# Kernel optimization log

Measured on AMD Instinct MI355X. Metric: run time of the kernel, lower is better.

## Reference

```python
import jax, jax.numpy as jnp
import numpy as np

N, L, D, H = 4, 2048, 1024, 16
HD = D // H  # head_dim = 64


def setup_inputs() -> dict:
    key = jax.random.key(0)
    ks = jax.random.split(key, 6)
    x = jax.random.normal(ks[0], (N, L, D), dtype=jnp.float32)
    mask = jax.random.randint(ks[1], (N, L), 0, 2).astype(bool)
    W_qkv = jax.random.normal(ks[2], (3 * D, D), dtype=jnp.float32) * (1.0 / np.sqrt(D))
    b_qkv = jax.random.normal(ks[3], (3 * D,), dtype=jnp.float32) * 0.02
    W_out = jax.random.normal(ks[4], (D, D), dtype=jnp.float32) * (1.0 / np.sqrt(D))
    b_out = jax.random.normal(ks[5], (D,), dtype=jnp.float32) * 0.02
    return {"x": x, "mask": mask, "W_qkv": W_qkv, "b_qkv": b_qkv,
            "W_out": W_out, "b_out": b_out}


def reference(x, mask, W_qkv, b_qkv, W_out, b_out):
    # qkv projection: torch Linear is y = x @ W.T + b
    qkv = jnp.einsum('nld,ed->nle', x, W_qkv) + b_qkv          # [N, L, 3D]
    q, k, v = jnp.split(qkv, 3, axis=-1)                        # each [N, L, D]
    # [N, L, D] -> [N, H, L, HD]
    to_heads = lambda t: t.reshape(N, L, H, HD).transpose(0, 2, 1, 3)
    q, k, v = to_heads(q), to_heads(k), to_heads(v)
    scale = 1.0 / np.sqrt(HD)
    scores = jnp.einsum('nhqd,nhkd->nhqk', q, k) * scale        # [N, H, L, L]
    # faithful to source: masked_fill where mask is True -> -1e9
    scores = jnp.where(mask[:, None, None, :], -1e9, scores)
    attn = jax.nn.softmax(scores, axis=-1)                      # dropout = identity (eval)
    out = jnp.einsum('nhqk,nhkd->nhqd', attn, v)                # [N, H, L, HD]
    out = out.transpose(0, 2, 1, 3).reshape(N, L, D)
    return jnp.einsum('nld,ed->nle', out, W_out) + b_out
```

## Files before the change

### kernel.cpp

```cpp
#include <hip/hip_runtime.h>
#include <hip/hip_bf16.h>
#include <cmath>

#define NB   4
#define LL   2048
#define DD   1024
#define HH   16
#define HD   64

typedef __bf16 bf16;
typedef __bf16 bf16x4 __attribute__((ext_vector_type(4)));
typedef __bf16 bf16x8 __attribute__((ext_vector_type(8)));
typedef float  f32x4  __attribute__((ext_vector_type(4)));
typedef float  f32x8  __attribute__((ext_vector_type(8)));

__device__ __forceinline__ void gload16(void* lds_base, const void* gsrc) {
    __builtin_amdgcn_global_load_lds(
        (const __attribute__((address_space(1))) unsigned int*)gsrc,
        (__attribute__((address_space(3))) unsigned int*)lds_base, 16, 0, 0);
}

__global__ __launch_bounds__(1024) void mask_prep(const unsigned char* __restrict__ mraw,
                                                  float* __restrict__ maskB) {
    __shared__ int anyOdd;
    if (threadIdx.x == 0) anyOdd = 0;
    __syncthreads();
    const int base = blockIdx.x * 1024;
    const int i = base + threadIdx.x;
    if ((i & 3) != 0 && mraw[i] != 0) atomicOr(&anyOdd, 1);
    __syncthreads();
    const bool isBytes = (anyOdd != 0);
    int v = isBytes ? (int)mraw[i] : ((const int*)mraw)[i];
    maskB[i] = v ? -1.4426950408889634e9f : -12.0f;
}

__global__ __launch_bounds__(256) void cast_f32_bf16(const float* __restrict__ src,
                                                     bf16* __restrict__ dst, int n8) {
    const int i = blockIdx.x * 256 + threadIdx.x;
    if (i >= n8) return;
    const float4* s = (const float4*)src + (size_t)i * 2;
    float4 a = s[0], b = s[1];
    bf16x8 o;
    o[0] = (bf16)a.x; o[1] = (bf16)a.y; o[2] = (bf16)a.z; o[3] = (bf16)a.w;
    o[4] = (bf16)b.x; o[5] = (bf16)b.y; o[6] = (bf16)b.z; o[7] = (bf16)b.w;
    *((bf16x8*)dst + i) = o;
}

template <int EPI>
__global__ __launch_bounds__(256) void gemm_mfma(const bf16* __restrict__ A,
                                                 const bf16* __restrict__ B,
                                                 const float* __restrict__ bias,
                                                 void* __restrict__ C0v,
                                                 void* __restrict__ C1v,
                                                 void* __restrict__ C2v,
                                                 int M, int N, int K) {
    __shared__ __attribute__((aligned(16))) char As[128 * 64];
    __shared__ __attribute__((aligned(16))) char Bs[128 * 64];

    const int tid = threadIdx.x;
    const int wave = tid >> 6;
    const int lane = tid & 63;
    const int kl = lane & 15;
    const int h = lane >> 4;
    const int wm = wave >> 1;
    const int wn = wave & 1;
    const int m0 = blockIdx.y * 128;
    const int n0 = blockIdx.x * 128;

    f32x4 acc[4][4];
#pragma unroll
    for (int i = 0; i < 4; ++i)
#pragma unroll
        for (int j = 0; j < 4; ++j) acc[i][j] = (f32x4){0.f, 0.f, 0.f, 0.f};

    const int sr = wave * 16 + (lane >> 2);
    const int sc = (lane & 3) * 16;
    const char* A0 = (const char*)A + ((size_t)(m0 + sr) * K) * 2 + sc;
    const char* A1 = (const char*)A + ((size_t)(m0 + 64 + sr) * K) * 2 + sc;
    const char* B0 = (const char*)B + ((size_t)(n0 + sr) * K) * 2 + sc;
    const char* B1 = (const char*)B + ((size_t)(n0 + 64 + sr) * K) * 2 + sc;
    char* AsD = As + wave * 1024;
    char* BsD = Bs + wave * 1024;

    for (int kt = 0; kt < K; kt += 32) {
        __syncthreads();
        gload16(AsD,        A0 + kt * 2);
        gload16(AsD + 4096, A1 + kt * 2);
        gload16(BsD,        B0 + kt * 2);
        gload16(BsD + 4096, B1 + kt * 2);
        asm volatile("s_waitcnt vmcnt(0)" ::: "memory");
        __syncthreads();

        bf16x8 a[4], b[4];
#pragma unroll
        for (int mt = 0; mt < 4; ++mt)
            a[mt] = *(const bf16x8*)(As + (wm * 64 + mt * 16 + kl) * 64 + h * 16);
#pragma unroll
        for (int nt = 0; nt < 4; ++nt)
            b[nt] = *(const bf16x8*)(Bs + (wn * 64 + nt * 16 + kl) * 64 + h * 16);
#pragma unroll
        for (int mt = 0; mt < 4; ++mt)
#pragma unroll
            for (int nt = 0; nt < 4; ++nt)
                acc[mt][nt] = __builtin_amdgcn_mfma_f32_16x16x32_bf16(a[mt], b[nt], acc[mt][nt], 0, 0, 0);
    }

    if (EPI == 1) {
        float* C0 = (float*)C0v;
#pragma unroll
        for (int mt = 0; mt < 4; ++mt) {
            const int mb = m0 + wm * 64 + mt * 16 + 4 * h;
#pragma unroll
            for (int nt = 0; nt < 4; ++nt) {
                const int n = n0 + wn * 64 + nt * 16 + kl;
                const float bv = bias[n];
#pragma unroll
                for (int r = 0; r < 4; ++r)
                    C0[(size_t)(mb + r) * N + n] = acc[mt][nt][r] + bv;
            }
        }
    } else {
        const int which = n0 >> 10;
        if (which < 2) {
            bf16* dst = (which == 0) ? (bf16*)C0v : (bf16*)C1v;
#pragma unroll
            for (int mt = 0; mt < 4; ++mt) {
                const int mb = m0 + wm * 64 + mt * 16 + 4 * h;
#pragma unroll
                for (int nt = 0; nt < 4; ++nt) {
                    const int gn = n0 + wn * 64 + nt * 16 + kl;
                    const float bv = bias[gn];
                    const int nn = gn & 1023;
                    const int hh = nn >> 6;
                    const int d = nn & 63;
#pragma unroll
                    for (int r = 0; r < 4; ++r) {
                        const int m = mb + r;
                        const int n_ = m >> 11;
                        const int l_ = m & 2047;
                        dst[((size_t)(n_ * HH + hh) * LL + l_) * HD + d] = (bf16)(acc[mt][nt][r] + bv);
                    }
                }
            }
        } else {
            bf16* dst = (bf16*)C2v;
#pragma unroll
            for (int mt = 0; mt < 4; ++mt) {
                const int mb = m0 + wm * 64 + mt * 16 + 4 * h;
                const int n_ = mb >> 11;
                const int l0 = mb & 2047;
#pragma unroll
                for (int nt = 0; nt < 4; ++nt) {
                    const int gn = n0 + wn * 64 + nt * 16 + kl;
                    const float bv = bias[gn];
                    const int nn = gn & 1023;
                    const int hh = nn >> 6;
                    const int d = nn & 63;
                    bf16x4 o4;
#pragma unroll
                    for (int r = 0; r < 4; ++r) o4[r] = (bf16)(acc[mt][nt][r] + bv);
                    *(bf16x4*)(dst + ((size_t)(n_ * HH + hh) * HD + d) * LL + l0) = o4;
                }
            }
        }
    }
}

#define SWZ3(row) ((((row) & 3) | ((((row) >> 3) & 1) << 2)) << 4)

__global__ __launch_bounds__(256) void attn_mfma(const bf16* __restrict__ Qg,
                                                 const bf16* __restrict__ Kg,
                                                 const bf16* __restrict__ VTg,
                                                 const float* __restrict__ maskB,
                                                 bf16* __restrict__ Oout) {
    __shared__ __attribute__((aligned(16))) char KtB0[8192];
    __shared__ __attribute__((aligned(16))) char KtB1[8192];
    __shared__ __attribute__((aligned(16))) char VtB0[8192];
    __shared__ __attribute__((aligned(16))) char VtB1[8192];

    const int tid = threadIdx.x;
    const int wave = tid >> 6;
    const int lane = tid & 63;
    const int kl = lane & 15;
    const int h = lane >> 4;

    const int f = blockIdx.x;
    const int qb = (f >> 3) & 15;
    const int bh = (f & 7) + ((f >> 7) << 3);
    const int n_ = bh >> 4;
    const int hh = bh & 15;
    const int q0 = qb * 128 + wave * 32;

    bf16x8 qf[2][2];
#pragma unroll
    for (int qt = 0; qt < 2; ++qt)
#pragma unroll
        for (int st = 0; st < 2; ++st)
            qf[qt][st] = *(const bf16x8*)(Qg + (((size_t)bh * LL + q0 + qt * 16 + kl) * HD + st * 32 + h * 8));

    f32x4 Oa[2][4];
    f32x4 Osum[2];
#pragma unroll
    for (int qt = 0; qt < 2; ++qt) {
        Osum[qt] = (f32x4){0.f, 0.f, 0.f, 0.f};
#pragma unroll
        for (int t = 0; t < 4; ++t) Oa[qt][t] = (f32x4){0.f, 0.f, 0.f, 0.f};
    }

    bf16x8 ones;
#pragma unroll
    for (int j = 0; j < 8; ++j) ones[j] = (bf16)1.0f;

    int koff[2][2][2];
#pragma unroll
    for (int c = 0; c < 2; ++c) {
        const int r1 = c * 32 + ((kl >> 2) << 3) + (kl & 3);
        const int r2 = r1 + 4;
#pragma unroll
        for (int st = 0; st < 2; ++st) {
            koff[c][0][st] = r1 * 128 + ((st * 64 + h * 16) ^ SWZ3(r1));
            koff[c][1][st] = r2 * 128 + ((st * 64 + h * 16) ^ SWZ3(r2));
        }
    }
    int voff[2][4];
#pragma unroll
    for (int c = 0; c < 2; ++c)
#pragma unroll
        for (int tt = 0; tt < 4; ++tt) {
            const int row = tt * 16 + kl;
            voff[c][tt] = row * 128 + ((c * 64 + h * 16) ^ SWZ3(row));
        }

    const int i0 = wave * 2 + 0, i1 = wave * 2 + 1;
    const int rA = i0 * 8 + (lane >> 3);
    const int rB = i1 * 8 + (lane >> 3);
    const int swA = ((lane & 7) << 4) ^ SWZ3(rA);
    const int swB = ((lane & 7) << 4) ^ SWZ3(rB);
    const char* Kb = (const char*)Kg + (size_t)bh * LL * 128;
    const char* Vb = (const char*)VTg + (size_t)bh * HD * (LL * 2);
    const char* kSA = Kb + (size_t)rA * 128 + swA;
    const char* kSB = Kb + (size_t)rB * 128 + swB;
    const char* vSA = Vb + (size_t)rA * 4096 + swA;
    const char* vSB = Vb + (size_t)rB * 4096 + swB;

    const float* mptr = maskB + n_ * LL + h * 8;
    const float scale = 0.18033688011f;

#define STAGE_TO(KT, VT, k0s)                                 \
    do {                                                      \
        gload16((KT) + i0 * 1024, kSA + (size_t)(k0s) * 128); \
        gload16((KT) + i1 * 1024, kSB + (size_t)(k0s) * 128); \
        gload16((VT) + i0 * 1024, vSA + (k0s) * 2);           \
        gload16((VT) + i1 * 1024, vSB + (k0s) * 2);           \
    } while (0)

#define LOADMK(MK, k0s)                                                    \
    do {                                                                   \
        _Pragma("unroll") for (int c = 0; c < 2; ++c)                      \
            _Pragma("unroll") for (int f2 = 0; f2 < 2; ++f2)               \
                MK[c][f2] = *(const f32x4*)(mptr + (k0s) + c * 32 + f2 * 4); \
    } while (0)

#define COMPUTE(KT, VT, MK)                                                            \
    do {                                                                               \
        bf16x8 kf[2][2][2], vf[2][4];                                                  \
        _Pragma("unroll") for (int c = 0; c < 2; ++c) {                                \
            _Pragma("unroll") for (int fr = 0; fr < 2; ++fr)                           \
                _Pragma("unroll") for (int st = 0; st < 2; ++st)                       \
                    kf[c][fr][st] = *(const bf16x8*)((KT) + koff[c][fr][st]);          \
            _Pragma("unroll") for (int tt = 0; tt < 4; ++tt)                           \
                vf[c][tt] = *(const bf16x8*)((VT) + voff[c][tt]);                      \
        }                                                                              \
        asm volatile("s_waitcnt lgkmcnt(0)" ::: "memory");                             \
        __builtin_amdgcn_sched_barrier(0);                                             \
        _Pragma("unroll") for (int qt = 0; qt < 2; ++qt) {                             \
            f32x4 sv[2][2];                                                            \
            __builtin_amdgcn_s_setprio(1);                                             \
            _Pragma("unroll") for (int c = 0; c < 2; ++c)                              \
                _Pragma("unroll") for (int fr = 0; fr < 2; ++fr) {                     \
                    f32x4 z = {0.f, 0.f, 0.f, 0.f};                                    \
                    f32x4 a = __builtin_amdgcn_mfma_f32_16x16x32_bf16(kf[c][fr][0],    \
                                                         qf[qt][0], z, 0, 0, 0);       \
                    sv[c][fr] = __builtin_amdgcn_mfma_f32_16x16x32_bf16(kf[c][fr][1],  \
                                                         qf[qt][1], a, 0, 0, 0);       \
                }                                                                      \
            __builtin_amdgcn_s_setprio(0);                                             \
            bf16x8 pa[2];                                                              \
            _Pragma("unroll") for (int c = 0; c < 2; ++c) {                            \
                f32x8 pf;                                                              \
                _Pragma("unroll") for (int f2 = 0; f2 < 2; ++f2) {                     \
                    f32x4 s = sv[c][f2] * scale + MK[c][f2];                           \
                    _Pragma("unroll") for (int r = 0; r < 4; ++r)                      \
                        pf[f2 * 4 + r] = __builtin_amdgcn_exp2f(s[r]);                 \
                }                                                                      \
                pa[c] = __builtin_convertvector(pf, bf16x8);                           \
            }                                                                          \
            __builtin_amdgcn_s_setprio(1);                                             \
            Osum[qt] = __builtin_amdgcn_mfma_f32_16x16x32_bf16(pa[0], ones,            \
                                                               Osum[qt], 0, 0, 0);     \
            Osum[qt] = __builtin_amdgcn_mfma_f32_16x16x32_bf16(pa[1], ones,            \
                                                               Osum[qt], 0, 0, 0);     \
            _Pragma("unroll") for (int c = 0; c < 2; ++c)                              \
                _Pragma("unroll") for (int tt = 0; tt < 4; ++tt)                       \
                    Oa[qt][tt] = __builtin_amdgcn_mfma_f32_16x16x32_bf16(pa[c],        \
                                                 vf[c][tt], Oa[qt][tt], 0, 0, 0);      \
            __builtin_amdgcn_s_setprio(0);                                             \
        }                                                                              \
    } while (0)

    f32x4 mkA[2][2], mkB[2][2];

    LOADMK(mkA, 0);
    STAGE_TO(KtB0, VtB0, 0);
    asm volatile("s_waitcnt vmcnt(0)" ::: "memory");
    __builtin_amdgcn_s_barrier();

    for (int t = 0; t < 32; t += 2) {
        STAGE_TO(KtB1, VtB1, (t + 1) * 64);
        __builtin_amdgcn_sched_barrier(0);
        LOADMK(mkB, (t + 1) * 64);
        COMPUTE(KtB0, VtB0, mkA);
        asm volatile("s_waitcnt vmcnt(4)" ::: "memory");
        __builtin_amdgcn_s_barrier();

        if (t + 2 < 32) {
            STAGE_TO(KtB0, VtB0, (t + 2) * 64);
            __builtin_amdgcn_sched_barrier(0);
            LOADMK(mkA, (t + 2) * 64);
            COMPUTE(KtB1, VtB1, mkB);
            asm volatile("s_waitcnt vmcnt(4)" ::: "memory");
            __builtin_amdgcn_s_barrier();
        } else {
            COMPUTE(KtB1, VtB1, mkB);
        }
    }

#pragma unroll
    for (int qt = 0; qt < 2; ++qt) {
#pragma unroll
        for (int r = 0; r < 4; ++r) {
            const float inv = 1.0f / Osum[qt][r];
            const int qrow = q0 + qt * 16 + h * 4 + r;
#pragma unroll
            for (int tt = 0; tt < 4; ++tt)
                Oout[((size_t)n_ * LL + qrow) * DD + hh * HD + tt * 16 + kl] =
                    (bf16)(Oa[qt][tt][r] * inv);
        }
    }
#undef STAGE_TO
#undef LOADMK
#undef COMPUTE
}

extern "C" void kernel_launch(void* const* d_in, const int* in_sizes, int n_in,
                              void* d_out, int out_size, void* d_ws, size_t ws_size,
                              hipStream_t stream) {
    const float* x     = (const float*)d_in[0];
    const void*  mask  = d_in[1];
    const float* W_qkv = (const float*)d_in[2];
    const float* b_qkv = (const float*)d_in[3];
    const float* W_out = (const float*)d_in[4];
    const float* b_out = (const float*)d_in[5];
    float* out = (float*)d_out;

    char* ws = (char*)d_ws;
    float* maskB = (float*)ws;
    bf16*  xb    = (bf16*)(ws + (1ull  << 20));
    bf16*  wqb   = (bf16*)(ws + (18ull << 20));
    bf16*  wob   = (bf16*)(ws + (25ull << 20));
    bf16*  qb    = (bf16*)(ws + (28ull << 20));
    bf16*  kb    = (bf16*)(ws + (45ull << 20));
    bf16*  vtb   = (bf16*)(ws + (62ull << 20));
    bf16*  attnb = (bf16*)(ws + (79ull << 20));

    mask_prep<<<8, 1024, 0, stream>>>((const unsigned char*)mask, maskB);

    cast_f32_bf16<<<(NB * LL * DD / 8) / 256, 256, 0, stream>>>(x, xb, NB * LL * DD / 8);
    cast_f32_bf16<<<(3 * DD * DD / 8) / 256, 256, 0, stream>>>(W_qkv, wqb, 3 * DD * DD / 8);
    cast_f32_bf16<<<(DD * DD / 8) / 256, 256, 0, stream>>>(W_out, wob, DD * DD / 8);

    gemm_mfma<0><<<dim3(3 * DD / 128, NB * LL / 128), 256, 0, stream>>>(
        xb, wqb, b_qkv, qb, kb, vtb, NB * LL, 3 * DD, DD);

    attn_mfma<<<1024, 256, 0, stream>>>(qb, kb, vtb, maskB, attnb);

    gemm_mfma<1><<<dim3(DD / 128, NB * LL / 128), 256, 0, stream>>>(
        attnb, wob, b_out, out, nullptr, nullptr, NB * LL, DD, DD);
}
```

Baseline: 214.4 us.

## Widen attention blocks to 8 waves and split K/V LDS read waits

The attention kernel now runs 512 threads per block covering 256 query rows, so each staged K/V tile serves twice as many queries. Each wave now issues one K load and one V load per stage instead of two of each. Inside COMPUTE, the K fragment reads come first and only they are waited on (lgkmcnt(8)) before the QK MFMAs and exp; the V reads are awaited later, before the PV MFMAs. The s_setprio hints are removed. The larger blocks halve the grid to 512 blocks, which may reduce occupancy and load balance across CUs.

Result: faster. 208.1 us (-2.9%).

```diff
diff --git a/kernel.cpp b/kernel.cpp
--- a/kernel.cpp
+++ b/kernel.cpp
@@ -168,7 +168,7 @@
 
 #define SWZ3(row) ((((row) & 3) | ((((row) >> 3) & 1) << 2)) << 4)
 
-__global__ __launch_bounds__(256) void attn_mfma(const bf16* __restrict__ Qg,
+__global__ __launch_bounds__(512) void attn_mfma(const bf16* __restrict__ Qg,
                                                  const bf16* __restrict__ Kg,
                                                  const bf16* __restrict__ VTg,
                                                  const float* __restrict__ maskB,
@@ -185,11 +185,11 @@
     const int h = lane >> 4;
 
     const int f = blockIdx.x;
-    const int qb = (f >> 3) & 15;
-    const int bh = (f & 7) + ((f >> 7) << 3);
+    const int qb = (f >> 3) & 7;
+    const int bh = (f & 7) | ((f >> 6) << 3);
     const int n_ = bh >> 4;
     const int hh = bh & 15;
-    const int q0 = qb * 128 + wave * 32;
+    const int q0 = qb * 256 + wave * 32;
 
     bf16x8 qf[2][2];
 #pragma unroll
@@ -231,51 +231,45 @@
             voff[c][tt] = row * 128 + ((c * 64 + h * 16) ^ SWZ3(row));
         }
 
-    const int i0 = wave * 2 + 0, i1 = wave * 2 + 1;
-    const int rA = i0 * 8 + (lane >> 3);
-    const int rB = i1 * 8 + (lane >> 3);
+    const int rA = wave * 8 + (lane >> 3);
     const int swA = ((lane & 7) << 4) ^ SWZ3(rA);
-    const int swB = ((lane & 7) << 4) ^ SWZ3(rB);
     const char* Kb = (const char*)Kg + (size_t)bh * LL * 128;
     const char* Vb = (const char*)VTg + (size_t)bh * HD * (LL * 2);
     const char* kSA = Kb + (size_t)rA * 128 + swA;
-    const char* kSB = Kb + (size_t)rB * 128 + swB;
     const char* vSA = Vb + (size_t)rA * 4096 + swA;
-    const char* vSB = Vb + (size_t)rB * 4096 + swB;
 
     const float* mptr = maskB + n_ * LL + h * 8;
     const float scale = 0.18033688011f;
 
-#define STAGE_TO(KT, VT, k0s)                                 \
-    do {                                                      \
-        gload16((KT) + i0 * 1024, kSA + (size_t)(k0s) * 128); \
-        gload16((KT) + i1 * 1024, kSB + (size_t)(k0s) * 128); \
-        gload16((VT) + i0 * 1024, vSA + (k0s) * 2);           \
-        gload16((VT) + i1 * 1024, vSB + (k0s) * 2);           \
+#define STAGE_TO(KT, VT, k0s)                                   \
+    do {                                                        \
+        gload16((KT) + wave * 1024, kSA + (size_t)(k0s) * 128); \
+        gload16((VT) + wave * 1024, vSA + (k0s) * 2);           \
     } while (0)
 
-#define LOADMK(MK, k0s)                                                    \
-    do {                                                                   \
-        _Pragma("unroll") for (int c = 0; c < 2; ++c)                      \
-            _Pragma("unroll") for (int f2 = 0; f2 < 2; ++f2)               \
+#define LOADMK(MK, k0s)                                                      \
+    do {                                                                     \
+        _Pragma("unroll") for (int c = 0; c < 2; ++c)                        \
+            _Pragma("unroll") for (int f2 = 0; f2 < 2; ++f2)                 \
                 MK[c][f2] = *(const f32x4*)(mptr + (k0s) + c * 32 + f2 * 4); \
     } while (0)
 
 #define COMPUTE(KT, VT, MK)                                                            \
     do {                                                                               \
         bf16x8 kf[2][2][2], vf[2][4];                                                  \
-        _Pragma("unroll") for (int c = 0; c < 2; ++c) {                                \
+        _Pragma("unroll") for (int c = 0; c < 2; ++c)                                  \
             _Pragma("unroll") for (int fr = 0; fr < 2; ++fr)                           \
                 _Pragma("unroll") for (int st = 0; st < 2; ++st)                       \
                     kf[c][fr][st] = *(const bf16x8*)((KT) + koff[c][fr][st]);          \
+        __builtin_amdgcn_sched_barrier(0);             \
+        _Pragma("unroll") for (int c = 0; c < 2; ++c)                                  \
             _Pragma("unroll") for (int tt = 0; tt < 4; ++tt)                           \
                 vf[c][tt] = *(const bf16x8*)((VT) + voff[c][tt]);                      \
-        }                                                                              \
-        asm volatile("s_waitcnt lgkmcnt(0)" ::: "memory");                             \
+        asm volatile("s_waitcnt lgkmcnt(8)" ::: "memory");                \
         __builtin_amdgcn_sched_barrier(0);                                             \
+        bf16x8 pa[2][2];                                                               \
         _Pragma("unroll") for (int qt = 0; qt < 2; ++qt) {                             \
             f32x4 sv[2][2];                                                            \
-            __builtin_amdgcn_s_setprio(1);                                             \
             _Pragma("unroll") for (int c = 0; c < 2; ++c)                              \
                 _Pragma("unroll") for (int fr = 0; fr < 2; ++fr) {                     \
                     f32x4 z = {0.f, 0.f, 0.f, 0.f};                                    \
@@ -284,8 +278,6 @@
                     sv[c][fr] = __builtin_amdgcn_mfma_f32_16x16x32_bf16(kf[c][fr][1],  \
                                                          qf[qt][1], a, 0, 0, 0);       \
                 }                                                                      \
-            __builtin_amdgcn_s_setprio(0);                                             \
-            bf16x8 pa[2];                                                              \
             _Pragma("unroll") for (int c = 0; c < 2; ++c) {                            \
                 f32x8 pf;                                                              \
                 _Pragma("unroll") for (int f2 = 0; f2 < 2; ++f2) {                     \
@@ -293,18 +285,20 @@
                     _Pragma("unroll") for (int r = 0; r < 4; ++r)                      \
                         pf[f2 * 4 + r] = __builtin_amdgcn_exp2f(s[r]);                 \
                 }                                                                      \
-                pa[c] = __builtin_convertvector(pf, bf16x8);                           \
+                pa[qt][c] = __builtin_convertvector(pf, bf16x8);                       \
             }                                                                          \
-            __builtin_amdgcn_s_setprio(1);                                             \
-            Osum[qt] = __builtin_amdgcn_mfma_f32_16x16x32_bf16(pa[0], ones,            \
+        }                                                                              \
+        asm volatile("s_waitcnt lgkmcnt(0)" ::: "memory");                \
+        __builtin_amdgcn_sched_barrier(0);                                             \
+        _Pragma("unroll") for (int qt = 0; qt < 2; ++qt) {                             \
+            Osum[qt] = __builtin_amdgcn_mfma_f32_16x16x32_bf16(pa[qt][0], ones,        \
                                                                Osum[qt], 0, 0, 0);     \
-            Osum[qt] = __builtin_amdgcn_mfma_f32_16x16x32_bf16(pa[1], ones,            \
+            Osum[qt] = __builtin_amdgcn_mfma_f32_16x16x32_bf16(pa[qt][1], ones,        \
                                                                Osum[qt], 0, 0, 0);     \
             _Pragma("unroll") for (int c = 0; c < 2; ++c)                              \
                 _Pragma("unroll") for (int tt = 0; tt < 4; ++tt)                       \
-                    Oa[qt][tt] = __builtin_amdgcn_mfma_f32_16x16x32_bf16(pa[c],        \
+                    Oa[qt][tt] = __builtin_amdgcn_mfma_f32_16x16x32_bf16(pa[qt][c],    \
                                                  vf[c][tt], Oa[qt][tt], 0, 0, 0);      \
-            __builtin_amdgcn_s_setprio(0);                                             \
         }                                                                              \
     } while (0)
 
@@ -382,7 +376,7 @@
     gemm_mfma<0><<<dim3(3 * DD / 128, NB * LL / 128), 256, 0, stream>>>(
         xb, wqb, b_qkv, qb, kb, vtb, NB * LL, 3 * DD, DD);
 
-    attn_mfma<<<1024, 256, 0, stream>>>(qb, kb, vtb, maskB, attnb);
+    attn_mfma<<<512, 512, 0, stream>>>(qb, kb, vtb, maskB, attnb);
 
     gemm_mfma<1><<<dim3(DD / 128, NB * LL / 128), 256, 0, stream>>>(
         attnb, wob, b_out, out, nullptr, nullptr, NB * LL, DD, DD);
```

## Double attention query tile per wave, stage mask in LDS, batch PV phase

Applied to the files above, without the earlier changes.

Each wave now handles 64 query rows instead of 32 (256 per block), halving the grid to 512 blocks so each K/V tile loaded into LDS is reused across twice as many queries. The per-batch mask row is preloaded once into LDS instead of being read from global memory every iteration. The compute is restructured to run all QK^T and softmax for four query tiles first, then load V fragments and do all PV MFMAs, and the setprio hints are dropped. The cost is higher register pressure, fewer blocks for occupancy, and a stricter vmcnt(0) wait each step.

Measured after the change: 219.4 us. +2.4%, slower.

```diff
diff --git a/kernel.cpp b/kernel.cpp
--- a/kernel.cpp
+++ b/kernel.cpp
@@ -177,6 +177,7 @@
     __shared__ __attribute__((aligned(16))) char KtB1[8192];
     __shared__ __attribute__((aligned(16))) char VtB0[8192];
     __shared__ __attribute__((aligned(16))) char VtB1[8192];
+    __shared__ __attribute__((aligned(16))) char MaskL[8192];
 
     const int tid = threadIdx.x;
     const int wave = tid >> 6;
@@ -185,23 +186,23 @@
     const int h = lane >> 4;
 
     const int f = blockIdx.x;
-    const int qb = (f >> 3) & 15;
-    const int bh = (f & 7) + ((f >> 7) << 3);
+    const int qb = (f >> 3) & 7;
+    const int bh = (f & 7) | ((f >> 6) << 3);
     const int n_ = bh >> 4;
     const int hh = bh & 15;
-    const int q0 = qb * 128 + wave * 32;
-
-    bf16x8 qf[2][2];
-#pragma unroll
-    for (int qt = 0; qt < 2; ++qt)
+    const int q0 = qb * 256 + wave * 64;
+
+    bf16x8 qf[4][2];
+#pragma unroll
+    for (int qt = 0; qt < 4; ++qt)
 #pragma unroll
         for (int st = 0; st < 2; ++st)
             qf[qt][st] = *(const bf16x8*)(Qg + (((size_t)bh * LL + q0 + qt * 16 + kl) * HD + st * 32 + h * 8));
 
-    f32x4 Oa[2][4];
-    f32x4 Osum[2];
-#pragma unroll
-    for (int qt = 0; qt < 2; ++qt) {
+    f32x4 Oa[4][4];
+    f32x4 Osum[4];
+#pragma unroll
+    for (int qt = 0; qt < 4; ++qt) {
         Osum[qt] = (f32x4){0.f, 0.f, 0.f, 0.f};
 #pragma unroll
         for (int t = 0; t < 4; ++t) Oa[qt][t] = (f32x4){0.f, 0.f, 0.f, 0.f};
@@ -243,8 +244,8 @@
     const char* vSA = Vb + (size_t)rA * 4096 + swA;
     const char* vSB = Vb + (size_t)rB * 4096 + swB;
 
-    const float* mptr = maskB + n_ * LL + h * 8;
     const float scale = 0.18033688011f;
+    const char* mlds = MaskL + h * 32;
 
 #define STAGE_TO(KT, VT, k0s)                                 \
     do {                                                      \
@@ -254,28 +255,22 @@
         gload16((VT) + i1 * 1024, vSB + (k0s) * 2);           \
     } while (0)
 
-#define LOADMK(MK, k0s)                                                    \
-    do {                                                                   \
-        _Pragma("unroll") for (int c = 0; c < 2; ++c)                      \
-            _Pragma("unroll") for (int f2 = 0; f2 < 2; ++f2)               \
-                MK[c][f2] = *(const f32x4*)(mptr + (k0s) + c * 32 + f2 * 4); \
-    } while (0)
-
-#define COMPUTE(KT, VT, MK)                                                            \
+#define COMPUTE(KT, VT, MOFF)                                                          \
     do {                                                                               \
-        bf16x8 kf[2][2][2], vf[2][4];                                                  \
-        _Pragma("unroll") for (int c = 0; c < 2; ++c) {                                \
+        bf16x8 kf[2][2][2];                                                            \
+        _Pragma("unroll") for (int c = 0; c < 2; ++c)                                  \
             _Pragma("unroll") for (int fr = 0; fr < 2; ++fr)                           \
                 _Pragma("unroll") for (int st = 0; st < 2; ++st)                       \
                     kf[c][fr][st] = *(const bf16x8*)((KT) + koff[c][fr][st]);          \
-            _Pragma("unroll") for (int tt = 0; tt < 4; ++tt)                           \
-                vf[c][tt] = *(const bf16x8*)((VT) + voff[c][tt]);                      \
-        }                                                                              \
-        asm volatile("s_waitcnt lgkmcnt(0)" ::: "memory");                             \
         __builtin_amdgcn_sched_barrier(0);                                             \
-        _Pragma("unroll") for (int qt = 0; qt < 2; ++qt) {                             \
+        f32x4 mk[2][2];                                                                \
+        _Pragma("unroll") for (int c = 0; c < 2; ++c)                                  \
+            _Pragma("unroll") for (int f2 = 0; f2 < 2; ++f2)                           \
+                mk[c][f2] = *(const f32x4*)(mlds + (MOFF) + c * 128 + f2 * 16);        \
+        __builtin_amdgcn_sched_barrier(0);                                             \
+        bf16x8 pa[4][2];                                                               \
+        _Pragma("unroll") for (int qt = 0; qt < 4; ++qt) {                             \
             f32x4 sv[2][2];                                                            \
-            __builtin_amdgcn_s_setprio(1);                                             \
             _Pragma("unroll") for (int c = 0; c < 2; ++c)                              \
                 _Pragma("unroll") for (int fr = 0; fr < 2; ++fr) {                     \
                     f32x4 z = {0.f, 0.f, 0.f, 0.f};                                    \
@@ -284,33 +279,38 @@
                     sv[c][fr] = __builtin_amdgcn_mfma_f32_16x16x32_bf16(kf[c][fr][1],  \
                                                          qf[qt][1], a, 0, 0, 0);       \
                 }                                                                      \
-            __builtin_amdgcn_s_setprio(0);                                             \
-            bf16x8 pa[2];                                                              \
             _Pragma("unroll") for (int c = 0; c < 2; ++c) {                            \
                 f32x8 pf;                                                              \
                 _Pragma("unroll") for (int f2 = 0; f2 < 2; ++f2) {                     \
-                    f32x4 s = sv[c][f2] * scale + MK[c][f2];                           \
+                    f32x4 s = sv[c][f2] * scale + mk[c][f2];                           \
                     _Pragma("unroll") for (int r = 0; r < 4; ++r)                      \
                         pf[f2 * 4 + r] = __builtin_amdgcn_exp2f(s[r]);                 \
                 }                                                                      \
-                pa[c] = __builtin_convertvector(pf, bf16x8);                           \
+                pa[qt][c] = __builtin_convertvector(pf, bf16x8);                       \
             }                                                                          \
-            __builtin_amdgcn_s_setprio(1);                                             \
-            Osum[qt] = __builtin_amdgcn_mfma_f32_16x16x32_bf16(pa[0], ones,            \
+        }                                                                              \
+        __builtin_amdgcn_sched_barrier(0);                                             \
+        bf16x8 vf[2][4];                                                               \
+        _Pragma("unroll") for (int c = 0; c < 2; ++c)                                  \
+            _Pragma("unroll") for (int tt = 0; tt < 4; ++tt)                           \
+                vf[c][tt] = *(const bf16x8*)((VT) + voff[c][tt]);                      \
+        _Pragma("unroll") for (int qt = 0; qt < 4; ++qt) {                             \
+            Osum[qt] = __builtin_amdgcn_mfma_f32_16x16x32_bf16(pa[qt][0], ones,        \
                                                                Osum[qt], 0, 0, 0);     \
-            Osum[qt] = __builtin_amdgcn_mfma_f32_16x16x32_bf16(pa[1], ones,            \
+            Osum[qt] = __builtin_amdgcn_mfma_f32_16x16x32_bf16(pa[qt][1], ones,        \
                                                                Osum[qt], 0, 0, 0);     \
             _Pragma("unroll") for (int c = 0; c < 2; ++c)                              \
                 _Pragma("unroll") for (int tt = 0; tt < 4; ++tt)                       \
-                    Oa[qt][tt] = __builtin_amdgcn_mfma_f32_16x16x32_bf16(pa[c],        \
+                    Oa[qt][tt] = __builtin_amdgcn_mfma_f32_16x16x32_bf16(pa[qt][c],    \
                                                  vf[c][tt], Oa[qt][tt], 0, 0, 0);      \
-            __builtin_amdgcn_s_setprio(0);                                             \
         }                                                                              \
     } while (0)
 
-    f32x4 mkA[2][2], mkB[2][2];
-
-    LOADMK(mkA, 0);
+    {
+        const char* msrc = (const char*)(maskB + n_ * LL) + wave * 2048 + lane * 16;
+        gload16(MaskL + wave * 2048,        msrc);
+        gload16(MaskL + wave * 2048 + 1024, msrc + 1024);
+    }
     STAGE_TO(KtB0, VtB0, 0);
     asm volatile("s_waitcnt vmcnt(0)" ::: "memory");
     __builtin_amdgcn_s_barrier();
@@ -318,25 +318,23 @@
     for (int t = 0; t < 32; t += 2) {
         STAGE_TO(KtB1, VtB1, (t + 1) * 64);
         __builtin_amdgcn_sched_barrier(0);
-        LOADMK(mkB, (t + 1) * 64);
-        COMPUTE(KtB0, VtB0, mkA);
-        asm volatile("s_waitcnt vmcnt(4)" ::: "memory");
+        COMPUTE(KtB0, VtB0, t * 256);
+        asm volatile("s_waitcnt vmcnt(0)" ::: "memory");
         __builtin_amdgcn_s_barrier();
 
         if (t + 2 < 32) {
             STAGE_TO(KtB0, VtB0, (t + 2) * 64);
             __builtin_amdgcn_sched_barrier(0);
-            LOADMK(mkA, (t + 2) * 64);
-            COMPUTE(KtB1, VtB1, mkB);
-            asm volatile("s_waitcnt vmcnt(4)" ::: "memory");
+            COMPUTE(KtB1, VtB1, (t + 1) * 256);
+            asm volatile("s_waitcnt vmcnt(0)" ::: "memory");
             __builtin_amdgcn_s_barrier();
         } else {
-            COMPUTE(KtB1, VtB1, mkB);
-        }
-    }
-
-#pragma unroll
-    for (int qt = 0; qt < 2; ++qt) {
+            COMPUTE(KtB1, VtB1, (t + 1) * 256);
+        }
+    }
+
+#pragma unroll
+    for (int qt = 0; qt < 4; ++qt) {
 #pragma unroll
         for (int r = 0; r < 4; ++r) {
             const float inv = 1.0f / Osum[qt][r];
@@ -348,7 +346,6 @@
         }
     }
 #undef STAGE_TO
-#undef LOADMK
 #undef COMPUTE
 }
 
@@ -382,7 +379,7 @@
     gemm_mfma<0><<<dim3(3 * DD / 128, NB * LL / 128), 256, 0, stream>>>(
         xb, wqb, b_qkv, qb, kb, vtb, NB * LL, 3 * DD, DD);
 
-    attn_mfma<<<1024, 256, 0, stream>>>(qb, kb, vtb, maskB, attnb);
+    attn_mfma<<<512, 256, 0, stream>>>(qb, kb, vtb, maskB, attnb);
 
     gemm_mfma<1><<<dim3(DD / 128, NB * LL / 128), 256, 0, stream>>>(
         attnb, wob, b_out, out, nullptr, nullptr, NB * LL, DD, DD);
```
